# Kernel tuning notes

Hardware: AMD Instinct MI355X
Metric: run time of the kernel (lower is better)

Reference implementation:

```python
import jax, jax.numpy as jnp
import numpy as np

B, P, D = 8, 196, 768       # batch, patches per image, hidden
H, DH = 12, 64              # heads, head dim (H*DH == D)
L = 4                       # GAT layers
THRESH = 0.1                # GraphGenerator similarity threshold
SLOPE = 0.2                 # LeakyReLU negative slope (DGL GATConv default)
NEG = -1e9


def setup_inputs() -> dict:
    key = jax.random.key(0)
    k0, k1, k2, k3, k4 = jax.random.split(key, 5)
    l_feat = jax.random.normal(k0, (B, P, D), jnp.float32)
    r_feat = jax.random.normal(k1, (B, P, D), jnp.float32)
    W = jax.random.normal(k2, (L, D, H * DH), jnp.float32) / np.float32(np.sqrt(D))
    a_src = jax.random.normal(k3, (L, H, DH), jnp.float32) / np.float32(np.sqrt(DH))
    a_dst = jax.random.normal(k4, (L, H, DH), jnp.float32) / np.float32(np.sqrt(DH))
    b = jnp.zeros((L, H * DH), jnp.float32)
    return dict(l_feat=l_feat, r_feat=r_feat, W=W, a_src=a_src, a_dst=a_dst, b=b)


def _leaky(x):
    return jax.nn.leaky_relu(x, SLOPE)


def _gat_layer_bipartite(h, Wl, a_s, a_d, bias, mask_rl, Nl):
    # Graph: edges l->r where mask_rl[r, l] is True, plus a self loop on every node.
    # l-nodes therefore only see themselves (alpha = 1).
    N = h.shape[0]
    z = (h @ Wl).reshape(N, H, DH)                      # [N, H, DH]
    el = jnp.einsum('nhd,hd->nh', z, a_s)               # src score
    er = jnp.einsum('nhd,hd->nh', z, a_d)               # dst score
    zl, zr = z[:Nl], z[Nl:]
    cross = _leaky(el[:Nl][None, :, :] + er[Nl:][:, None, :])   # [Nr, Nl, H]
    cross = jnp.where(mask_rl[..., None], cross, NEG)
    self_r = _leaky(el[Nl:] + er[Nl:])                   # [Nr, H] self-loop logit
    logits = jnp.concatenate([cross, self_r[:, None, :]], axis=1)  # [Nr, Nl+1, H]
    alpha = jax.nn.softmax(logits, axis=1)
    out_r = jnp.einsum('rlh,lhd->rhd', alpha[:, :Nl], zl) + alpha[:, Nl][..., None] * zr
    out = jnp.concatenate([zl, out_r], axis=0)           # l-nodes: identity (self loop)
    return out.reshape(N, H * DH) + bias


def _gat_layer_pool(h, Wl, a_s, a_d, bias):
    # Graph from _gather: every node -> first node of its P-block (col = img_node
    # repeat_interleave) plus add_self_loop. The root's self edge thus appears TWICE,
    # giving it multiplicity 2 in the edge softmax. Non-root nodes: self loop only.
    N = h.shape[0]
    G = N // P
    z = (h @ Wl).reshape(G, P, H, DH)
    el = jnp.einsum('gphd,hd->gph', z, a_s)
    er = jnp.einsum('gphd,hd->gph', z, a_d)
    logits = _leaky(el + er[:, :1, :])                   # [G, P, H], dst = node 0
    logc = jnp.log(jnp.where(jnp.arange(P) == 0, 2.0, 1.0)).astype(h.dtype)
    alpha = jax.nn.softmax(logits + logc[None, :, None], axis=1)
    pooled = jnp.einsum('gph,gphd->ghd', alpha, z)       # root aggregation
    out = z.at[:, 0].set(pooled)                         # others keep self value
    return out.reshape(N, H * DH) + bias


def _gat(h, W, a_src, a_dst, b, layer_fn):
    for i in range(L):
        h = layer_fn(h, W[i], a_src[i], a_dst[i], b[i])
        if i < L - 1:
            h = jax.nn.elu(h)
    return h


def reference(l_feat, r_feat, W, a_src, a_dst, b):
    node_l = l_feat.reshape(-1, D)
    node_r = r_feat.reshape(-1, D)
    Nl = node_l.shape[0]
    # GraphGenerator: cosine-similarity threshold graph (edges l -> r)
    nl = node_l / jnp.linalg.norm(node_l, axis=-1, keepdims=True)
    nr = node_r / jnp.linalg.norm(node_r, axis=-1, keepdims=True)
    mask_rl = (nr @ nl.T) > THRESH                       # [Nr, Nl]
    h = jnp.concatenate([node_l, node_r], axis=0)        # [2*B*P, D]
    h = _gat(h, W, a_src, a_dst, b,
             lambda x, w, s, d, bb: _gat_layer_bipartite(x, w, s, d, bb, mask_rl, Nl))
    # second GAT pass on the pooling graph, then index_select the per-image roots
    h = _gat(h, W, a_src, a_dst, b, _gat_layer_pool)
    img = h[::P]                                         # img_node = arange(0, N, P)
    return img[:B], img[B:]                              # (node_feat_l, node_feat_r)
```

## Files before the change

kernel.cpp:

```cpp
#include <hip/hip_runtime.h>
#include <math.h>

#define NL    1568
#define NTOT  3136
#define DD    768
#define NH    12
#define DHD   64
#define WPR   49
#define MAXDEG 64
#define NKSTEP 24
#define LOG2F_ 0.69314718055994530942f

typedef _Float16 h8 __attribute__((ext_vector_type(8)));
typedef float f32x4 __attribute__((ext_vector_type(4)));
#define MFMA16(a, b, c) __builtin_amdgcn_mfma_f32_16x16x32_f16(a, b, c, 0, 0, 0)

__device__ __forceinline__ float leaky(float x) { return x > 0.f ? x : 0.2f * x; }

__device__ __forceinline__ void gld16(const _Float16* g, _Float16* l) {
  __builtin_amdgcn_global_load_lds(
      (const __attribute__((address_space(1))) void*)g,
      (__attribute__((address_space(3))) void*)l, 16, 0, 0);
}

__global__ __launch_bounds__(192) void conv_init(const float* __restrict__ lf, const float* __restrict__ rf,
                                                 _Float16* __restrict__ hi, _Float16* __restrict__ lo,
                                                 float* __restrict__ norms) {
  int n = blockIdx.x;
  int t = threadIdx.x;
  const float* src = (n < NL) ? lf + (size_t)n * DD : rf + (size_t)(n - NL) * DD;
  float4 v = reinterpret_cast<const float4*>(src)[t];
  _Float16 a0 = (_Float16)v.x, a1 = (_Float16)v.y, a2 = (_Float16)v.z, a3 = (_Float16)v.w;
  typedef _Float16 h4v __attribute__((ext_vector_type(4)));
  h4v hv = {a0, a1, a2, a3};
  h4v lv = {(_Float16)((v.x - (float)a0) * 2048.f), (_Float16)((v.y - (float)a1) * 2048.f),
            (_Float16)((v.z - (float)a2) * 2048.f), (_Float16)((v.w - (float)a3) * 2048.f)};
  size_t idx = (size_t)n * (DD / 4) + t;
  reinterpret_cast<h4v*>(hi)[idx] = hv;
  reinterpret_cast<h4v*>(lo)[idx] = lv;
  float s = v.x * v.x + v.y * v.y + v.z * v.z + v.w * v.w;
  #pragma unroll
  for (int o = 32; o; o >>= 1) s += __shfl_xor(s, o);
  __shared__ float red[3];
  if ((t & 63) == 0) red[t >> 6] = s;
  __syncthreads();
  if (t == 0) norms[n] = sqrtf(red[0] + red[1] + red[2]);
}

__global__ __launch_bounds__(256) void transp_W(const float* __restrict__ W, _Float16* __restrict__ Wthi) {
  __shared__ float tile[32][33];
  int kt = blockIdx.x * 32, nt = blockIdx.y * 32, i = blockIdx.z;
  int tx = threadIdx.x & 31, ty = threadIdx.x >> 5;
  const float* Wp = W + ((size_t)i * DD + kt) * DD + nt;
  #pragma unroll
  for (int p = 0; p < 4; ++p) tile[ty + p * 8][tx] = Wp[(size_t)(ty + p * 8) * DD + tx];
  __syncthreads();
  _Float16* oh = Wthi + ((size_t)i * DD + nt) * DD + kt;
  #pragma unroll
  for (int p = 0; p < 4; ++p) {
    int nn = ty + p * 8;
    oh[(size_t)nn * DD + tx] = (_Float16)tile[tx][nn];
  }
}

__global__ __launch_bounds__(256) void gemm_mfma(const _Float16* __restrict__ Ahi,
                                                 const _Float16* __restrict__ Bhi,
                                                 const float* __restrict__ a_s, const float* __restrict__ a_d,
                                                 const float* __restrict__ bias, float* __restrict__ C,
                                                 float* __restrict__ el, float* __restrict__ er,
                                                 _Float16* __restrict__ ohhi,
                                                 int do_elu, int mode) {
  __shared__ _Float16 sm[2][2][2048];
  int t = threadIdx.x;
  int xcd = blockIdx.x & 7, pos = blockIdx.x >> 3;
  int orig = (xcd < 4 ? xcd * 74 : 4 * 74 + (xcd - 4) * 73) + pos;
  int bx = orig / 12, by = orig % 12;
  int m0 = bx * 64, n0 = by * 64;

  int rl = t >> 2;
  int kq_src = (t & 3) ^ ((t >> 3) & 3);
  size_t aoff = (size_t)(m0 + rl) * DD + kq_src * 8;
  size_t boff = (size_t)(n0 + rl) * DD + kq_src * 8;
  const _Float16* pAhi = Ahi + aoff;
  const _Float16* pBhi = Bhi + boff;
  int ch = (t >> 6) * 512;

  int ln = t & 63, wv = t >> 6;
  int fr = ln & 15, kg = ln >> 4;
  int kq8 = (kg ^ ((fr >> 1) & 3)) * 8;
  int aRead = (wv * 16 + fr) * 32 + kq8;

  f32x4 zero = {0.f, 0.f, 0.f, 0.f};
  f32x4 acc1[4];
  #pragma unroll
  for (int cg = 0; cg < 4; ++cg) acc1[cg] = zero;

  gld16(pAhi, &sm[0][0][ch]);
  gld16(pBhi, &sm[0][1][ch]);
  __syncthreads();

  for (int step = 0; step < NKSTEP; ++step) {
    int buf = step & 1;
    if (step < NKSTEP - 1) {
      int kb = (step + 1) * 32;
      gld16(pAhi + kb, &sm[buf ^ 1][0][ch]);
      gld16(pBhi + kb, &sm[buf ^ 1][1][ch]);
    }
    h8 ah = *reinterpret_cast<const h8*>(&sm[buf][0][aRead]);
    #pragma unroll
    for (int cg = 0; cg < 4; ++cg) {
      int bRead = (cg * 16 + fr) * 32 + kq8;
      h8 bh = *reinterpret_cast<const h8*>(&sm[buf][1][bRead]);
      acc1[cg] = MFMA16(ah, bh, acc1[cg]);
    }
    __syncthreads();
  }

  int head = by;
  int orow = m0 + wv * 16 + kg * 4;
  #pragma unroll
  for (int i = 0; i < 4; ++i) {
    int r = orow + i;
    bool wh = (mode == 0) ? (r < NL) : (r % 196 != 0);
    #pragma unroll
    for (int cg = 0; cg < 4; ++cg) {
      int c = n0 + cg * 16 + fr;
      float z = acc1[cg][i];
      C[(size_t)r * DD + c] = z;
      if (wh) {
        float o = z + bias[c];
        if (do_elu) o = o > 0.f ? o : expm1f(o);
        ohhi[(size_t)r * DD + c] = (_Float16)o;
      }
    }
  }
  float asv[4], adv[4];
  #pragma unroll
  for (int cg = 0; cg < 4; ++cg) {
    asv[cg] = a_s[head * DHD + cg * 16 + fr];
    adv[cg] = a_d[head * DHD + cg * 16 + fr];
  }
  #pragma unroll
  for (int i = 0; i < 4; ++i) {
    float s1 = 0.f, s2 = 0.f;
    #pragma unroll
    for (int cg = 0; cg < 4; ++cg) {
      s1 = fmaf(acc1[cg][i], asv[cg], s1);
      s2 = fmaf(acc1[cg][i], adv[cg], s2);
    }
    #pragma unroll
    for (int o = 1; o < 16; o <<= 1) {
      s1 += __shfl_xor(s1, o);
      s2 += __shfl_xor(s2, o);
    }
    if (fr == 0) {
      el[(size_t)(orow + i) * NH + head] = s1;
      er[(size_t)(orow + i) * NH + head] = s2;
    }
  }
}

__global__ __launch_bounds__(256) void mask_mfma(const _Float16* __restrict__ Hhi, const _Float16* __restrict__ Hlo,
                                                 const float* __restrict__ norms, unsigned* __restrict__ mask) {
  __shared__ _Float16 sm[2][4][2048];
  __shared__ unsigned mw[64][2];
  int t = threadIdx.x;
  int r0 = blockIdx.x * 64, l0 = blockIdx.y * 64;

  int rl = t >> 2;
  int kq_src = (t & 3) ^ ((t >> 3) & 3);
  int ra = r0 + rl; if (ra >= NL) ra = NL - 1;
  int la = l0 + rl; if (la >= NL) la = NL - 1;
  size_t aoff = (size_t)(NL + ra) * DD + kq_src * 8;
  size_t boff = (size_t)la * DD + kq_src * 8;
  const _Float16* pAhi = Hhi + aoff;
  const _Float16* pAlo = Hlo + aoff;
  const _Float16* pBhi = Hhi + boff;
  const _Float16* pBlo = Hlo + boff;
  int ch = (t >> 6) * 512;

  int ln = t & 63, wv = t >> 6;
  int fr = ln & 15, kg = ln >> 4;
  int kq8 = (kg ^ ((fr >> 1) & 3)) * 8;
  int aRead = (wv * 16 + fr) * 32 + kq8;

  f32x4 zero = {0.f, 0.f, 0.f, 0.f};
  f32x4 acc1[4], acc2[4];
  #pragma unroll
  for (int cg = 0; cg < 4; ++cg) { acc1[cg] = zero; acc2[cg] = zero; }
  if (t < 128) mw[t >> 1][t & 1] = 0u;

  gld16(pAhi, &sm[0][0][ch]);
  gld16(pAlo, &sm[0][1][ch]);
  gld16(pBhi, &sm[0][2][ch]);
  gld16(pBlo, &sm[0][3][ch]);
  __syncthreads();

  for (int step = 0; step < NKSTEP; ++step) {
    int buf = step & 1;
    if (step < NKSTEP - 1) {
      int kb = (step + 1) * 32;
      gld16(pAhi + kb, &sm[buf ^ 1][0][ch]);
      gld16(pAlo + kb, &sm[buf ^ 1][1][ch]);
      gld16(pBhi + kb, &sm[buf ^ 1][2][ch]);
      gld16(pBlo + kb, &sm[buf ^ 1][3][ch]);
    }
    h8 ah = *reinterpret_cast<const h8*>(&sm[buf][0][aRead]);
    h8 al = *reinterpret_cast<const h8*>(&sm[buf][1][aRead]);
    #pragma unroll
    for (int cg = 0; cg < 4; ++cg) {
      int bRead = (cg * 16 + fr) * 32 + kq8;
      h8 bh = *reinterpret_cast<const h8*>(&sm[buf][2][bRead]);
      h8 bl = *reinterpret_cast<const h8*>(&sm[buf][3][bRead]);
      acc1[cg] = MFMA16(ah, bh, acc1[cg]);
      acc2[cg] = MFMA16(ah, bl, acc2[cg]);
      acc2[cg] = MFMA16(al, bh, acc2[cg]);
    }
    __syncthreads();
  }

  int rloc = wv * 16 + kg * 4;
  float nrv[4];
  #pragma unroll
  for (int i = 0; i < 4; ++i) {
    int r = r0 + rloc + i;
    nrv[i] = norms[NL + (r < NL ? r : NL - 1)];
  }
  #pragma unroll
  for (int cg = 0; cg < 4; ++cg) {
    int lloc = cg * 16 + fr;
    int l = l0 + lloc;
    float nlv = norms[l < NL ? l : NL - 1];
    #pragma unroll
    for (int i = 0; i < 4; ++i) {
      int r = r0 + rloc + i;
      float dot = acc1[cg][i] + acc2[cg][i] * (1.f / 2048.f);
      if (r < NL && l < NL && dot > 0.1f * nrv[i] * nlv)
        atomicOr(&mw[rloc + i][lloc >> 5], 1u << (lloc & 31));
    }
  }
  __syncthreads();
  if (t < 128) {
    int rr = t >> 1, w = t & 1;
    int rg = r0 + rr, wg = blockIdx.y * 2 + w;
    if (rg < NL && wg < WPR) mask[(size_t)rg * WPR + wg] = mw[rr][w];
  }
}

__global__ __launch_bounds__(64) void build_csr(const unsigned* __restrict__ mask,
                                                int* __restrict__ nbr, int* __restrict__ deg) {
  int r = blockIdx.x * 64 + threadIdx.x;
  if (r >= NL) return;
  const unsigned* mr = mask + (size_t)r * WPR;
  int* out = nbr + (size_t)r * MAXDEG;
  int cnt = 0;
  #pragma unroll 7
  for (int w = 0; w < WPR; ++w) {
    unsigned m = mr[w];
    while (m) {
      int bpos = __ffs(m) - 1;
      m &= m - 1;
      if (cnt < MAXDEG) out[cnt] = w * 32 + bpos;
      ++cnt;
    }
  }
  deg[r] = cnt < MAXDEG ? cnt : MAXDEG;
}

__global__ __launch_bounds__(768) void bip_fused(const float* __restrict__ z, const float* __restrict__ el,
                                                 const float* __restrict__ er, const int* __restrict__ nbr,
                                                 const int* __restrict__ deg, const float* __restrict__ bias,
                                                 _Float16* __restrict__ ohhi,
                                                 int do_elu) {
  int r = blockIdx.x;
  int R = NL + r;
  int t = threadIdx.x;
  int dg = deg[r];
  __shared__ int nb_s[MAXDEG];
  __shared__ float wbuf[MAXDEG * NH];
  __shared__ float den_s[NH], wself_s[NH];
  if (t < dg) nb_s[t] = nbr[(size_t)r * MAXDEG + t];
  __syncthreads();
  if (t < dg * NH) {
    int j = t / NH, h2 = t - j * NH;
    wbuf[t] = el[(size_t)nb_s[j] * NH + h2];
  }
  __syncthreads();
  if (t < NH) {
    float er_r = er[(size_t)R * NH + t];
    float s = leaky(el[(size_t)R * NH + t] + er_r);
    float mx = s;
    for (int j = 0; j < dg; ++j) mx = fmaxf(mx, leaky(wbuf[j * NH + t] + er_r));
    float den = 0.f;
    for (int j = 0; j < dg; ++j) {
      float w = expf(leaky(wbuf[j * NH + t] + er_r) - mx);
      wbuf[j * NH + t] = w;
      den += w;
    }
    float ws = expf(s - mx);
    den_s[t] = den + ws;
    wself_s[t] = ws;
  }
  __syncthreads();
  int h2 = t >> 6;
  float acc = wself_s[h2] * z[(size_t)R * DD + t];
  for (int j = 0; j < dg; ++j)
    acc = fmaf(wbuf[j * NH + h2], z[(size_t)nb_s[j] * DD + t], acc);
  float o = acc / den_s[h2] + bias[t];
  if (do_elu) o = o > 0.f ? o : expm1f(o);
  ohhi[(size_t)R * DD + t] = (_Float16)o;
}

__global__ __launch_bounds__(256) void pool_attn2(const float* __restrict__ z, const float* __restrict__ el,
                                                  const float* __restrict__ er, const float* __restrict__ bias,
                                                  _Float16* __restrict__ ohhi,
                                                  float* __restrict__ root_out, int do_elu) {
  int g = blockIdx.x, h = blockIdx.y;
  int base = g * 196;
  int t = threadIdx.x;
  int w = t >> 6, d = t & 63;
  __shared__ float wb[196];
  __shared__ float red[4];
  __shared__ float accP[4][64];
  float er0 = er[(size_t)base * NH + h];
  float lg = -INFINITY;
  if (t < 196) {
    lg = leaky(el[(size_t)(base + t) * NH + h] + er0);
    if (t == 0) lg += LOG2F_;
  }
  float m = lg;
  #pragma unroll
  for (int o = 32; o; o >>= 1) m = fmaxf(m, __shfl_xor(m, o));
  if ((t & 63) == 0) red[w] = m;
  __syncthreads();
  float mx = fmaxf(fmaxf(red[0], red[1]), fmaxf(red[2], red[3]));
  float wgt = (t < 196) ? expf(lg - mx) : 0.f;
  if (t < 196) wb[t] = wgt;
  float dn = wgt;
  #pragma unroll
  for (int o = 32; o; o >>= 1) dn += __shfl_xor(dn, o);
  __syncthreads();
  if ((t & 63) == 0) red[w] = dn;
  __syncthreads();
  float den = red[0] + red[1] + red[2] + red[3];
  float acc = 0.f;
  int p0 = w * 49;
  #pragma unroll 7
  for (int p = p0; p < p0 + 49; ++p)
    acc = fmaf(wb[p], z[(size_t)(base + p) * DD + h * DHD + d], acc);
  accP[w][d] = acc;
  __syncthreads();
  if (w == 0) {
    float o = (accP[0][d] + accP[1][d] + accP[2][d] + accP[3][d]) / den + bias[h * DHD + d];
    if (do_elu) o = o > 0.f ? o : expm1f(o);
    int c = h * DHD + d;
    ohhi[(size_t)base * DD + c] = (_Float16)o;
    root_out[(size_t)g * DD + c] = o;
  }
}

extern "C" void kernel_launch(void* const* d_in, const int* in_sizes, int n_in,
                              void* d_out, int out_size, void* d_ws, size_t ws_size,
                              hipStream_t stream) {
  const float* l_feat = (const float*)d_in[0];
  const float* r_feat = (const float*)d_in[1];
  const float* W      = (const float*)d_in[2];
  const float* a_src  = (const float*)d_in[3];
  const float* a_dst  = (const float*)d_in[4];
  const float* b      = (const float*)d_in[5];
  float* out = (float*)d_out;

  float* z     = (float*)d_ws;
  float* el    = z + (size_t)NTOT * DD;
  float* er    = el + (size_t)NTOT * NH;
  float* norms = er + (size_t)NTOT * NH;
  float* hroot = norms + NTOT;
  unsigned* mask = (unsigned*)(hroot + 16 * DD);
  int* nbr = (int*)(mask + (size_t)NL * WPR);
  int* deg = nbr + (size_t)NL * MAXDEG;
  _Float16* hhiA = (_Float16*)(deg + NL);
  _Float16* hloA = hhiA + (size_t)NTOT * DD;
  _Float16* hhiB = hloA + (size_t)NTOT * DD;
  _Float16* Wthi = hhiB + (size_t)NTOT * DD;

  _Float16* hhi[2] = {hhiA, hhiB};

  conv_init<<<NTOT, 192, 0, stream>>>(l_feat, r_feat, hhiA, hloA, norms);
  transp_W<<<dim3(24, 24, 4), 256, 0, stream>>>(W, Wthi);
  mask_mfma<<<dim3(25, 25), 256, 0, stream>>>(hhiA, hloA, norms, mask);
  build_csr<<<(NL + 63) / 64, 64, 0, stream>>>(mask, nbr, deg);

  for (int i = 0; i < 4; ++i) {
    const float* bi = b + (size_t)i * DD;
    int do_elu = (i < 3) ? 1 : 0;
    int ib = i & 1, ob = (i + 1) & 1;
    gemm_mfma<<<588, 256, 0, stream>>>(hhi[ib],
        Wthi + (size_t)i * DD * DD,
        a_src + (size_t)i * NH * DHD, a_dst + (size_t)i * NH * DHD,
        bi, z, el, er, hhi[ob], do_elu, 0);
    bip_fused<<<NL, 768, 0, stream>>>(z, el, er, nbr, deg, bi, hhi[ob], do_elu);
  }

  for (int i = 0; i < 4; ++i) {
    const float* bi = b + (size_t)i * DD;
    int do_elu = (i < 3) ? 1 : 0;
    int L = 4 + i;
    int ib = L & 1, ob = (L + 1) & 1;
    gemm_mfma<<<588, 256, 0, stream>>>(hhi[ib],
        Wthi + (size_t)i * DD * DD,
        a_src + (size_t)i * NH * DHD, a_dst + (size_t)i * NH * DHD,
        bi, z, el, er, hhi[ob], do_elu, 1);
    pool_attn2<<<dim3(16, NH), 256, 0, stream>>>(z, el, er, bi, hhi[ob],
        (i == 3) ? out : hroot, do_elu);
  }
}
```

Baseline: 274.9 us.

## Use 32x32 MFMA with 64x128 GEMM tiles and store z in fp16

The projection GEMM now uses 32x32x16 MFMA instructions on a 64x128 output tile per block, halving the grid to 294 blocks and reusing each A tile across two heads. The projected features z are written as fp16 instead of fp32, which halves the write and read traffic in bip_fused and pool_attn2. The trade-off is fewer blocks for 256 CUs and lower precision in the aggregated z values.

```diff
diff --git a/kernel.cpp b/kernel.cpp
--- a/kernel.cpp
+++ b/kernel.cpp
@@ -13,7 +13,9 @@
 
 typedef _Float16 h8 __attribute__((ext_vector_type(8)));
 typedef float f32x4 __attribute__((ext_vector_type(4)));
+typedef float f32x16 __attribute__((ext_vector_type(16)));
 #define MFMA16(a, b, c) __builtin_amdgcn_mfma_f32_16x16x32_f16(a, b, c, 0, 0, 0)
+#define MFMA32(a, b, c) __builtin_amdgcn_mfma_f32_32x32x16_f16(a, b, c, 0, 0, 0)
 
 __device__ __forceinline__ float leaky(float x) { return x > 0.f ? x : 0.2f * x; }
 
@@ -66,96 +68,100 @@
 __global__ __launch_bounds__(256) void gemm_mfma(const _Float16* __restrict__ Ahi,
                                                  const _Float16* __restrict__ Bhi,
                                                  const float* __restrict__ a_s, const float* __restrict__ a_d,
-                                                 const float* __restrict__ bias, float* __restrict__ C,
+                                                 const float* __restrict__ bias,
+                                                 _Float16* __restrict__ zh,
                                                  float* __restrict__ el, float* __restrict__ er,
                                                  _Float16* __restrict__ ohhi,
                                                  int do_elu, int mode) {
-  __shared__ _Float16 sm[2][2][2048];
+  __shared__ _Float16 smA[2][2048];
+  __shared__ _Float16 smB[2][4096];
   int t = threadIdx.x;
   int xcd = blockIdx.x & 7, pos = blockIdx.x >> 3;
-  int orig = (xcd < 4 ? xcd * 74 : 4 * 74 + (xcd - 4) * 73) + pos;
-  int bx = orig / 12, by = orig % 12;
-  int m0 = bx * 64, n0 = by * 64;
+  int orig = (xcd < 6 ? xcd * 37 : 222 + (xcd - 6) * 36) + pos;
+  int bx = orig / 6, by = orig % 6;
+  int m0 = bx * 64, n0 = by * 128;
 
   int rl = t >> 2;
-  int kq_src = (t & 3) ^ ((t >> 3) & 3);
-  size_t aoff = (size_t)(m0 + rl) * DD + kq_src * 8;
-  size_t boff = (size_t)(n0 + rl) * DD + kq_src * 8;
-  const _Float16* pAhi = Ahi + aoff;
-  const _Float16* pBhi = Bhi + boff;
-  int ch = (t >> 6) * 512;
-
-  int ln = t & 63, wv = t >> 6;
-  int fr = ln & 15, kg = ln >> 4;
-  int kq8 = (kg ^ ((fr >> 1) & 3)) * 8;
-  int aRead = (wv * 16 + fr) * 32 + kq8;
-
-  f32x4 zero = {0.f, 0.f, 0.f, 0.f};
-  f32x4 acc1[4];
-  #pragma unroll
-  for (int cg = 0; cg < 4; ++cg) acc1[cg] = zero;
-
-  gld16(pAhi, &sm[0][0][ch]);
-  gld16(pBhi, &sm[0][1][ch]);
+  int kq_src = (t & 3) ^ ((rl >> 1) & 3);
+  const _Float16* pA  = Ahi + (size_t)(m0 + rl) * DD + kq_src * 8;
+  const _Float16* pB1 = Bhi + (size_t)(n0 + rl) * DD + kq_src * 8;
+  const _Float16* pB2 = Bhi + (size_t)(n0 + 64 + rl) * DD + kq_src * 8;
+  int w = t >> 6, l = t & 63;
+  int chA  = w * 512;
+  int chB2 = 2048 + w * 512;
+
+  int cl = l & 31, hi = l >> 5;
+  int rw = (w >> 1) * 32, cw = (w & 1) * 64;
+  int arow = rw + cl;
+  int aOff0 = arow * 32 + ((hi)     ^ ((arow >> 1) & 3)) * 8;
+  int aOff1 = arow * 32 + ((hi + 2) ^ ((arow >> 1) & 3)) * 8;
+  int brow0 = cw + cl, brow1 = cw + 32 + cl;
+  int bOff00 = brow0 * 32 + ((hi)     ^ ((brow0 >> 1) & 3)) * 8;
+  int bOff01 = brow0 * 32 + ((hi + 2) ^ ((brow0 >> 1) & 3)) * 8;
+  int bOff10 = brow1 * 32 + ((hi)     ^ ((brow1 >> 1) & 3)) * 8;
+  int bOff11 = brow1 * 32 + ((hi + 2) ^ ((brow1 >> 1) & 3)) * 8;
+
+  f32x16 acc0, acc1;
+  #pragma unroll
+  for (int i = 0; i < 16; ++i) { acc0[i] = 0.f; acc1[i] = 0.f; }
+
+  gld16(pA,  &smA[0][chA]);
+  gld16(pB1, &smB[0][chA]);
+  gld16(pB2, &smB[0][chB2]);
   __syncthreads();
 
   for (int step = 0; step < NKSTEP; ++step) {
     int buf = step & 1;
     if (step < NKSTEP - 1) {
       int kb = (step + 1) * 32;
-      gld16(pAhi + kb, &sm[buf ^ 1][0][ch]);
-      gld16(pBhi + kb, &sm[buf ^ 1][1][ch]);
-    }
-    h8 ah = *reinterpret_cast<const h8*>(&sm[buf][0][aRead]);
+      gld16(pA + kb,  &smA[buf ^ 1][chA]);
+      gld16(pB1 + kb, &smB[buf ^ 1][chA]);
+      gld16(pB2 + kb, &smB[buf ^ 1][chB2]);
+    }
+    h8 a0  = *reinterpret_cast<const h8*>(&smA[buf][aOff0]);
+    h8 a1  = *reinterpret_cast<const h8*>(&smA[buf][aOff1]);
+    h8 b00 = *reinterpret_cast<const h8*>(&smB[buf][bOff00]);
+    h8 b01 = *reinterpret_cast<const h8*>(&smB[buf][bOff01]);
+    h8 b10 = *reinterpret_cast<const h8*>(&smB[buf][bOff10]);
+    h8 b11 = *reinterpret_cast<const h8*>(&smB[buf][bOff11]);
+    acc0 = MFMA32(a0, b00, acc0);
+    acc1 = MFMA32(a0, b10, acc1);
+    acc0 = MFMA32(a1, b01, acc0);
+    acc1 = MFMA32(a1, b11, acc1);
+    __syncthreads();
+  }
+
+  int hd = by * 2 + (w & 1);
+  float as0 = a_s[hd * DHD + cl],      ad0 = a_d[hd * DHD + cl];
+  float as1 = a_s[hd * DHD + 32 + cl], ad1 = a_d[hd * DHD + 32 + cl];
+  int c0 = n0 + cw + cl, c1 = c0 + 32;
+  float bv0 = bias[c0], bv1 = bias[c1];
+  #pragma unroll
+  for (int r = 0; r < 16; ++r) {
+    int row = m0 + rw + (r & 3) + 8 * (r >> 2) + 4 * hi;
+    float z0 = acc0[r], z1 = acc1[r];
+    zh[(size_t)row * DD + c0] = (_Float16)z0;
+    zh[(size_t)row * DD + c1] = (_Float16)z1;
+    bool wh = (mode == 0) ? (row < NL) : (row % 196 != 0);
+    if (wh) {
+      float o0 = z0 + bv0, o1 = z1 + bv1;
+      if (do_elu) {
+        o0 = o0 > 0.f ? o0 : expm1f(o0);
+        o1 = o1 > 0.f ? o1 : expm1f(o1);
+      }
+      ohhi[(size_t)row * DD + c0] = (_Float16)o0;
+      ohhi[(size_t)row * DD + c1] = (_Float16)o1;
+    }
+    float s1 = z0 * as0 + z1 * as1;
+    float s2 = z0 * ad0 + z1 * ad1;
     #pragma unroll
-    for (int cg = 0; cg < 4; ++cg) {
-      int bRead = (cg * 16 + fr) * 32 + kq8;
-      h8 bh = *reinterpret_cast<const h8*>(&sm[buf][1][bRead]);
-      acc1[cg] = MFMA16(ah, bh, acc1[cg]);
-    }
-    __syncthreads();
-  }
-
-  int head = by;
-  int orow = m0 + wv * 16 + kg * 4;
-  #pragma unroll
-  for (int i = 0; i < 4; ++i) {
-    int r = orow + i;
-    bool wh = (mode == 0) ? (r < NL) : (r % 196 != 0);
-    #pragma unroll
-    for (int cg = 0; cg < 4; ++cg) {
-      int c = n0 + cg * 16 + fr;
-      float z = acc1[cg][i];
-      C[(size_t)r * DD + c] = z;
-      if (wh) {
-        float o = z + bias[c];
-        if (do_elu) o = o > 0.f ? o : expm1f(o);
-        ohhi[(size_t)r * DD + c] = (_Float16)o;
-      }
-    }
-  }
-  float asv[4], adv[4];
-  #pragma unroll
-  for (int cg = 0; cg < 4; ++cg) {
-    asv[cg] = a_s[head * DHD + cg * 16 + fr];
-    adv[cg] = a_d[head * DHD + cg * 16 + fr];
-  }
-  #pragma unroll
-  for (int i = 0; i < 4; ++i) {
-    float s1 = 0.f, s2 = 0.f;
-    #pragma unroll
-    for (int cg = 0; cg < 4; ++cg) {
-      s1 = fmaf(acc1[cg][i], asv[cg], s1);
-      s2 = fmaf(acc1[cg][i], adv[cg], s2);
-    }
-    #pragma unroll
-    for (int o = 1; o < 16; o <<= 1) {
+    for (int o = 1; o < 32; o <<= 1) {
       s1 += __shfl_xor(s1, o);
       s2 += __shfl_xor(s2, o);
     }
-    if (fr == 0) {
-      el[(size_t)(orow + i) * NH + head] = s1;
-      er[(size_t)(orow + i) * NH + head] = s2;
+    if (cl == 0) {
+      el[(size_t)row * NH + hd] = s1;
+      er[(size_t)row * NH + hd] = s2;
     }
   }
 }
@@ -267,7 +273,7 @@
   deg[r] = cnt < MAXDEG ? cnt : MAXDEG;
 }
 
-__global__ __launch_bounds__(768) void bip_fused(const float* __restrict__ z, const float* __restrict__ el,
+__global__ __launch_bounds__(768) void bip_fused(const _Float16* __restrict__ zh, const float* __restrict__ el,
                                                  const float* __restrict__ er, const int* __restrict__ nbr,
                                                  const int* __restrict__ deg, const float* __restrict__ bias,
                                                  _Float16* __restrict__ ohhi,
@@ -303,15 +309,15 @@
   }
   __syncthreads();
   int h2 = t >> 6;
-  float acc = wself_s[h2] * z[(size_t)R * DD + t];
+  float acc = wself_s[h2] * (float)zh[(size_t)R * DD + t];
   for (int j = 0; j < dg; ++j)
-    acc = fmaf(wbuf[j * NH + h2], z[(size_t)nb_s[j] * DD + t], acc);
+    acc = fmaf(wbuf[j * NH + h2], (float)zh[(size_t)nb_s[j] * DD + t], acc);
   float o = acc / den_s[h2] + bias[t];
   if (do_elu) o = o > 0.f ? o : expm1f(o);
   ohhi[(size_t)R * DD + t] = (_Float16)o;
 }
 
-__global__ __launch_bounds__(256) void pool_attn2(const float* __restrict__ z, const float* __restrict__ el,
+__global__ __launch_bounds__(256) void pool_attn2(const _Float16* __restrict__ zh, const float* __restrict__ el,
                                                   const float* __restrict__ er, const float* __restrict__ bias,
                                                   _Float16* __restrict__ ohhi,
                                                   float* __restrict__ root_out, int do_elu) {
@@ -347,7 +353,7 @@
   int p0 = w * 49;
   #pragma unroll 7
   for (int p = p0; p < p0 + 49; ++p)
-    acc = fmaf(wb[p], z[(size_t)(base + p) * DD + h * DHD + d], acc);
+    acc = fmaf(wb[p], (float)zh[(size_t)(base + p) * DD + h * DHD + d], acc);
   accP[w][d] = acc;
   __syncthreads();
   if (w == 0) {
@@ -370,8 +376,7 @@
   const float* b      = (const float*)d_in[5];
   float* out = (float*)d_out;
 
-  float* z     = (float*)d_ws;
-  float* el    = z + (size_t)NTOT * DD;
+  float* el    = (float*)d_ws;
   float* er    = el + (size_t)NTOT * NH;
   float* norms = er + (size_t)NTOT * NH;
   float* hroot = norms + NTOT;
@@ -382,6 +387,7 @@
   _Float16* hloA = hhiA + (size_t)NTOT * DD;
   _Float16* hhiB = hloA + (size_t)NTOT * DD;
   _Float16* Wthi = hhiB + (size_t)NTOT * DD;
+  _Float16* zh   = Wthi + (size_t)4 * DD * DD;
 
   _Float16* hhi[2] = {hhiA, hhiB};
 
@@ -394,11 +400,11 @@
     const float* bi = b + (size_t)i * DD;
     int do_elu = (i < 3) ? 1 : 0;
     int ib = i & 1, ob = (i + 1) & 1;
-    gemm_mfma<<<588, 256, 0, stream>>>(hhi[ib],
+    gemm_mfma<<<294, 256, 0, stream>>>(hhi[ib],
         Wthi + (size_t)i * DD * DD,
         a_src + (size_t)i * NH * DHD, a_dst + (size_t)i * NH * DHD,
-        bi, z, el, er, hhi[ob], do_elu, 0);
-    bip_fused<<<NL, 768, 0, stream>>>(z, el, er, nbr, deg, bi, hhi[ob], do_elu);
+        bi, zh, el, er, hhi[ob], do_elu, 0);
+    bip_fused<<<NL, 768, 0, stream>>>(zh, el, er, nbr, deg, bi, hhi[ob], do_elu);
   }
 
   for (int i = 0; i < 4; ++i) {
@@ -406,11 +412,11 @@
     int do_elu = (i < 3) ? 1 : 0;
     int L = 4 + i;
     int ib = L & 1, ob = (L + 1) & 1;
-    gemm_mfma<<<588, 256, 0, stream>>>(hhi[ib],
+    gemm_mfma<<<294, 256, 0, stream>>>(hhi[ib],
         Wthi + (size_t)i * DD * DD,
         a_src + (size_t)i * NH * DHD, a_dst + (size_t)i * NH * DHD,
-        bi, z, el, er, hhi[ob], do_elu, 1);
-    pool_attn2<<<dim3(16, NH), 256, 0, stream>>>(z, el, er, bi, hhi[ob],
+        bi, zh, el, er, hhi[ob], do_elu, 1);
+    pool_attn2<<<dim3(16, NH), 256, 0, stream>>>(zh, el, er, bi, hhi[ob],
         (i == 3) ? out : hroot, do_elu);
   }
 }
```

After: 308.2 us. +12.1%, slower.

## Store projected features as fp16 and use 64-wide K tiles in GEMM

Applied to the files above, without the earlier changes.

The GEMM now loads 64-wide K slices per stage, with a new XOR swizzle, which halves the number of loop iterations and barriers. The projected feature matrix z is written in half precision instead of fp32. The bipartite and pooling attention kernels read this fp16 z, which halves the bytes written by the GEMM and gathered per neighbour. The trade-off is extra rounding error in z and higher LDS use per block.

```diff
diff --git a/kernel.cpp b/kernel.cpp
--- a/kernel.cpp
+++ b/kernel.cpp
@@ -9,6 +9,7 @@
 #define WPR   49
 #define MAXDEG 64
 #define NKSTEP 24
+#define NK64   12
 #define LOG2F_ 0.69314718055994530942f
 
 typedef _Float16 h8 __attribute__((ext_vector_type(8)));
@@ -66,58 +67,76 @@
 __global__ __launch_bounds__(256) void gemm_mfma(const _Float16* __restrict__ Ahi,
                                                  const _Float16* __restrict__ Bhi,
                                                  const float* __restrict__ a_s, const float* __restrict__ a_d,
-                                                 const float* __restrict__ bias, float* __restrict__ C,
+                                                 const float* __restrict__ bias,
+                                                 _Float16* __restrict__ zh,
                                                  float* __restrict__ el, float* __restrict__ er,
                                                  _Float16* __restrict__ ohhi,
                                                  int do_elu, int mode) {
-  __shared__ _Float16 sm[2][2][2048];
+  __shared__ _Float16 smA[2][4096];
+  __shared__ _Float16 smB[2][4096];
   int t = threadIdx.x;
   int xcd = blockIdx.x & 7, pos = blockIdx.x >> 3;
-  int orig = (xcd < 4 ? xcd * 74 : 4 * 74 + (xcd - 4) * 73) + pos;
+  int orig = (xcd < 4 ? xcd * 74 : 296 + (xcd - 4) * 73) + pos;
   int bx = orig / 12, by = orig % 12;
   int m0 = bx * 64, n0 = by * 64;
 
-  int rl = t >> 2;
-  int kq_src = (t & 3) ^ ((t >> 3) & 3);
-  size_t aoff = (size_t)(m0 + rl) * DD + kq_src * 8;
-  size_t boff = (size_t)(n0 + rl) * DD + kq_src * 8;
-  const _Float16* pAhi = Ahi + aoff;
-  const _Float16* pBhi = Bhi + boff;
-  int ch = (t >> 6) * 512;
-
-  int ln = t & 63, wv = t >> 6;
-  int fr = ln & 15, kg = ln >> 4;
-  int kq8 = (kg ^ ((fr >> 1) & 3)) * 8;
-  int aRead = (wv * 16 + fr) * 32 + kq8;
+  int rs = t >> 3;
+  int kq0 = (t & 7) ^ (rs & 7);
+  const _Float16* pA0 = Ahi + (size_t)(m0 + rs) * DD + kq0 * 8;
+  const _Float16* pA1 = pA0 + (size_t)32 * DD;
+  const _Float16* pB0 = Bhi + (size_t)(n0 + rs) * DD + kq0 * 8;
+  const _Float16* pB1 = pB0 + (size_t)32 * DD;
+  int w = t >> 6, l = t & 63;
+  int ch0 = w * 512;
+  int ch1 = 2048 + w * 512;
+
+  int fr = l & 15, kg = l >> 4;
+  int aO[2], bO[4][2];
+  #pragma unroll
+  for (int kk = 0; kk < 2; ++kk) {
+    int arow = w * 16 + fr;
+    aO[kk] = arow * 64 + (((kk * 4 + kg) ^ (arow & 7)) * 8);
+    #pragma unroll
+    for (int cg = 0; cg < 4; ++cg) {
+      int brow = cg * 16 + fr;
+      bO[cg][kk] = brow * 64 + (((kk * 4 + kg) ^ (brow & 7)) * 8);
+    }
+  }
 
   f32x4 zero = {0.f, 0.f, 0.f, 0.f};
-  f32x4 acc1[4];
-  #pragma unroll
-  for (int cg = 0; cg < 4; ++cg) acc1[cg] = zero;
-
-  gld16(pAhi, &sm[0][0][ch]);
-  gld16(pBhi, &sm[0][1][ch]);
-  __syncthreads();
-
-  for (int step = 0; step < NKSTEP; ++step) {
+  f32x4 acc[4];
+  #pragma unroll
+  for (int cg = 0; cg < 4; ++cg) acc[cg] = zero;
+
+  gld16(pA0, &smA[0][ch0]);
+  gld16(pA1, &smA[0][ch1]);
+  gld16(pB0, &smB[0][ch0]);
+  gld16(pB1, &smB[0][ch1]);
+  __syncthreads();
+
+  for (int step = 0; step < NK64; ++step) {
     int buf = step & 1;
-    if (step < NKSTEP - 1) {
-      int kb = (step + 1) * 32;
-      gld16(pAhi + kb, &sm[buf ^ 1][0][ch]);
-      gld16(pBhi + kb, &sm[buf ^ 1][1][ch]);
-    }
-    h8 ah = *reinterpret_cast<const h8*>(&sm[buf][0][aRead]);
-    #pragma unroll
-    for (int cg = 0; cg < 4; ++cg) {
-      int bRead = (cg * 16 + fr) * 32 + kq8;
-      h8 bh = *reinterpret_cast<const h8*>(&sm[buf][1][bRead]);
-      acc1[cg] = MFMA16(ah, bh, acc1[cg]);
+    if (step < NK64 - 1) {
+      int kb = (step + 1) * 64;
+      gld16(pA0 + kb, &smA[buf ^ 1][ch0]);
+      gld16(pA1 + kb, &smA[buf ^ 1][ch1]);
+      gld16(pB0 + kb, &smB[buf ^ 1][ch0]);
+      gld16(pB1 + kb, &smB[buf ^ 1][ch1]);
+    }
+    #pragma unroll
+    for (int kk = 0; kk < 2; ++kk) {
+      h8 a = *reinterpret_cast<const h8*>(&smA[buf][aO[kk]]);
+      #pragma unroll
+      for (int cg = 0; cg < 4; ++cg) {
+        h8 b = *reinterpret_cast<const h8*>(&smB[buf][bO[cg][kk]]);
+        acc[cg] = MFMA16(a, b, acc[cg]);
+      }
     }
     __syncthreads();
   }
 
   int head = by;
-  int orow = m0 + wv * 16 + kg * 4;
+  int orow = m0 + w * 16 + kg * 4;
   #pragma unroll
   for (int i = 0; i < 4; ++i) {
     int r = orow + i;
@@ -125,8 +144,8 @@
     #pragma unroll
     for (int cg = 0; cg < 4; ++cg) {
       int c = n0 + cg * 16 + fr;
-      float z = acc1[cg][i];
-      C[(size_t)r * DD + c] = z;
+      float z = acc[cg][i];
+      zh[(size_t)r * DD + c] = (_Float16)z;
       if (wh) {
         float o = z + bias[c];
         if (do_elu) o = o > 0.f ? o : expm1f(o);
@@ -145,8 +164,8 @@
     float s1 = 0.f, s2 = 0.f;
     #pragma unroll
     for (int cg = 0; cg < 4; ++cg) {
-      s1 = fmaf(acc1[cg][i], asv[cg], s1);
-      s2 = fmaf(acc1[cg][i], adv[cg], s2);
+      s1 = fmaf(acc[cg][i], asv[cg], s1);
+      s2 = fmaf(acc[cg][i], adv[cg], s2);
     }
     #pragma unroll
     for (int o = 1; o < 16; o <<= 1) {
@@ -267,7 +286,7 @@
   deg[r] = cnt < MAXDEG ? cnt : MAXDEG;
 }
 
-__global__ __launch_bounds__(768) void bip_fused(const float* __restrict__ z, const float* __restrict__ el,
+__global__ __launch_bounds__(768) void bip_fused(const _Float16* __restrict__ zh, const float* __restrict__ el,
                                                  const float* __restrict__ er, const int* __restrict__ nbr,
                                                  const int* __restrict__ deg, const float* __restrict__ bias,
                                                  _Float16* __restrict__ ohhi,
@@ -303,15 +322,15 @@
   }
   __syncthreads();
   int h2 = t >> 6;
-  float acc = wself_s[h2] * z[(size_t)R * DD + t];
+  float acc = wself_s[h2] * (float)zh[(size_t)R * DD + t];
   for (int j = 0; j < dg; ++j)
-    acc = fmaf(wbuf[j * NH + h2], z[(size_t)nb_s[j] * DD + t], acc);
+    acc = fmaf(wbuf[j * NH + h2], (float)zh[(size_t)nb_s[j] * DD + t], acc);
   float o = acc / den_s[h2] + bias[t];
   if (do_elu) o = o > 0.f ? o : expm1f(o);
   ohhi[(size_t)R * DD + t] = (_Float16)o;
 }
 
-__global__ __launch_bounds__(256) void pool_attn2(const float* __restrict__ z, const float* __restrict__ el,
+__global__ __launch_bounds__(256) void pool_attn2(const _Float16* __restrict__ zh, const float* __restrict__ el,
                                                   const float* __restrict__ er, const float* __restrict__ bias,
                                                   _Float16* __restrict__ ohhi,
                                                   float* __restrict__ root_out, int do_elu) {
@@ -347,7 +366,7 @@
   int p0 = w * 49;
   #pragma unroll 7
   for (int p = p0; p < p0 + 49; ++p)
-    acc = fmaf(wb[p], z[(size_t)(base + p) * DD + h * DHD + d], acc);
+    acc = fmaf(wb[p], (float)zh[(size_t)(base + p) * DD + h * DHD + d], acc);
   accP[w][d] = acc;
   __syncthreads();
   if (w == 0) {
@@ -370,8 +389,7 @@
   const float* b      = (const float*)d_in[5];
   float* out = (float*)d_out;
 
-  float* z     = (float*)d_ws;
-  float* el    = z + (size_t)NTOT * DD;
+  float* el    = (float*)d_ws;
   float* er    = el + (size_t)NTOT * NH;
   float* norms = er + (size_t)NTOT * NH;
   float* hroot = norms + NTOT;
@@ -382,6 +400,7 @@
   _Float16* hloA = hhiA + (size_t)NTOT * DD;
   _Float16* hhiB = hloA + (size_t)NTOT * DD;
   _Float16* Wthi = hhiB + (size_t)NTOT * DD;
+  _Float16* zh   = Wthi + (size_t)4 * DD * DD;
 
   _Float16* hhi[2] = {hhiA, hhiB};
 
@@ -397,8 +416,8 @@
     gemm_mfma<<<588, 256, 0, stream>>>(hhi[ib],
         Wthi + (size_t)i * DD * DD,
         a_src + (size_t)i * NH * DHD, a_dst + (size_t)i * NH * DHD,
-        bi, z, el, er, hhi[ob], do_elu, 0);
-    bip_fused<<<NL, 768, 0, stream>>>(z, el, er, nbr, deg, bi, hhi[ob], do_elu);
+        bi, zh, el, er, hhi[ob], do_elu, 0);
+    bip_fused<<<NL, 768, 0, stream>>>(zh, el, er, nbr, deg, bi, hhi[ob], do_elu);
   }
 
   for (int i = 0; i < 4; ++i) {
@@ -409,8 +428,8 @@
     gemm_mfma<<<588, 256, 0, stream>>>(hhi[ib],
         Wthi + (size_t)i * DD * DD,
         a_src + (size_t)i * NH * DHD, a_dst + (size_t)i * NH * DHD,
-        bi, z, el, er, hhi[ob], do_elu, 1);
-    pool_attn2<<<dim3(16, NH), 256, 0, stream>>>(z, el, er, bi, hhi[ob],
+        bi, zh, el, er, hhi[ob], do_elu, 1);
+    pool_attn2<<<dim3(16, NH), 256, 0, stream>>>(zh, el, er, bi, hhi[ob],
         (i == 3) ? out : hroot, do_elu);
   }
 }
```

Result: slower. 281.1 us (+2.3%).

## Store GAT projections in fp16 and use single-pass fp16 mask with fp32 fallback

Applied to the files above, without the earlier changes.

The similarity-mask GEMM now uses only the fp16 high part instead of the hi/lo split, which halves its MFMA and load work. Pairs whose fp16 dot product lands within 0.5 of the threshold are recomputed exactly in fp32 straight from the input features. Separately, the projected features z are stored as fp16 instead of fp32, which halves the write traffic in the GEMM and the gather traffic in the attention kernels. The cost is lower precision in the aggregated outputs, and a fallback path whose per-element work varies and can diverge within a wavefront.

```diff
diff --git a/kernel.cpp b/kernel.cpp
--- a/kernel.cpp
+++ b/kernel.cpp
@@ -24,20 +24,14 @@
 }
 
 __global__ __launch_bounds__(192) void conv_init(const float* __restrict__ lf, const float* __restrict__ rf,
-                                                 _Float16* __restrict__ hi, _Float16* __restrict__ lo,
-                                                 float* __restrict__ norms) {
+                                                 _Float16* __restrict__ hi, float* __restrict__ norms) {
   int n = blockIdx.x;
   int t = threadIdx.x;
   const float* src = (n < NL) ? lf + (size_t)n * DD : rf + (size_t)(n - NL) * DD;
   float4 v = reinterpret_cast<const float4*>(src)[t];
-  _Float16 a0 = (_Float16)v.x, a1 = (_Float16)v.y, a2 = (_Float16)v.z, a3 = (_Float16)v.w;
   typedef _Float16 h4v __attribute__((ext_vector_type(4)));
-  h4v hv = {a0, a1, a2, a3};
-  h4v lv = {(_Float16)((v.x - (float)a0) * 2048.f), (_Float16)((v.y - (float)a1) * 2048.f),
-            (_Float16)((v.z - (float)a2) * 2048.f), (_Float16)((v.w - (float)a3) * 2048.f)};
-  size_t idx = (size_t)n * (DD / 4) + t;
-  reinterpret_cast<h4v*>(hi)[idx] = hv;
-  reinterpret_cast<h4v*>(lo)[idx] = lv;
+  h4v hv = {(_Float16)v.x, (_Float16)v.y, (_Float16)v.z, (_Float16)v.w};
+  reinterpret_cast<h4v*>(hi)[(size_t)n * (DD / 4) + t] = hv;
   float s = v.x * v.x + v.y * v.y + v.z * v.z + v.w * v.w;
   #pragma unroll
   for (int o = 32; o; o >>= 1) s += __shfl_xor(s, o);
@@ -66,14 +60,15 @@
 __global__ __launch_bounds__(256) void gemm_mfma(const _Float16* __restrict__ Ahi,
                                                  const _Float16* __restrict__ Bhi,
                                                  const float* __restrict__ a_s, const float* __restrict__ a_d,
-                                                 const float* __restrict__ bias, float* __restrict__ C,
+                                                 const float* __restrict__ bias,
+                                                 _Float16* __restrict__ zh,
                                                  float* __restrict__ el, float* __restrict__ er,
                                                  _Float16* __restrict__ ohhi,
                                                  int do_elu, int mode) {
   __shared__ _Float16 sm[2][2][2048];
   int t = threadIdx.x;
   int xcd = blockIdx.x & 7, pos = blockIdx.x >> 3;
-  int orig = (xcd < 4 ? xcd * 74 : 4 * 74 + (xcd - 4) * 73) + pos;
+  int orig = (xcd < 4 ? xcd * 74 : 296 + (xcd - 4) * 73) + pos;
   int bx = orig / 12, by = orig % 12;
   int m0 = bx * 64, n0 = by * 64;
 
@@ -91,9 +86,9 @@
   int aRead = (wv * 16 + fr) * 32 + kq8;
 
   f32x4 zero = {0.f, 0.f, 0.f, 0.f};
-  f32x4 acc1[4];
-  #pragma unroll
-  for (int cg = 0; cg < 4; ++cg) acc1[cg] = zero;
+  f32x4 acc[4];
+  #pragma unroll
+  for (int cg = 0; cg < 4; ++cg) acc[cg] = zero;
 
   gld16(pAhi, &sm[0][0][ch]);
   gld16(pBhi, &sm[0][1][ch]);
@@ -111,7 +106,7 @@
     for (int cg = 0; cg < 4; ++cg) {
       int bRead = (cg * 16 + fr) * 32 + kq8;
       h8 bh = *reinterpret_cast<const h8*>(&sm[buf][1][bRead]);
-      acc1[cg] = MFMA16(ah, bh, acc1[cg]);
+      acc[cg] = MFMA16(ah, bh, acc[cg]);
     }
     __syncthreads();
   }
@@ -125,8 +120,8 @@
     #pragma unroll
     for (int cg = 0; cg < 4; ++cg) {
       int c = n0 + cg * 16 + fr;
-      float z = acc1[cg][i];
-      C[(size_t)r * DD + c] = z;
+      float z = acc[cg][i];
+      zh[(size_t)r * DD + c] = (_Float16)z;
       if (wh) {
         float o = z + bias[c];
         if (do_elu) o = o > 0.f ? o : expm1f(o);
@@ -145,8 +140,8 @@
     float s1 = 0.f, s2 = 0.f;
     #pragma unroll
     for (int cg = 0; cg < 4; ++cg) {
-      s1 = fmaf(acc1[cg][i], asv[cg], s1);
-      s2 = fmaf(acc1[cg][i], adv[cg], s2);
+      s1 = fmaf(acc[cg][i], asv[cg], s1);
+      s2 = fmaf(acc[cg][i], adv[cg], s2);
     }
     #pragma unroll
     for (int o = 1; o < 16; o <<= 1) {
@@ -160,9 +155,10 @@
   }
 }
 
-__global__ __launch_bounds__(256) void mask_mfma(const _Float16* __restrict__ Hhi, const _Float16* __restrict__ Hlo,
+__global__ __launch_bounds__(256) void mask_mfma(const _Float16* __restrict__ Hhi,
+                                                 const float* __restrict__ lf, const float* __restrict__ rf,
                                                  const float* __restrict__ norms, unsigned* __restrict__ mask) {
-  __shared__ _Float16 sm[2][4][2048];
+  __shared__ _Float16 sm[2][2][2048];
   __shared__ unsigned mw[64][2];
   int t = threadIdx.x;
   int r0 = blockIdx.x * 64, l0 = blockIdx.y * 64;
@@ -171,12 +167,8 @@
   int kq_src = (t & 3) ^ ((t >> 3) & 3);
   int ra = r0 + rl; if (ra >= NL) ra = NL - 1;
   int la = l0 + rl; if (la >= NL) la = NL - 1;
-  size_t aoff = (size_t)(NL + ra) * DD + kq_src * 8;
-  size_t boff = (size_t)la * DD + kq_src * 8;
-  const _Float16* pAhi = Hhi + aoff;
-  const _Float16* pAlo = Hlo + aoff;
-  const _Float16* pBhi = Hhi + boff;
-  const _Float16* pBlo = Hlo + boff;
+  const _Float16* pA = Hhi + (size_t)(NL + ra) * DD + kq_src * 8;
+  const _Float16* pB = Hhi + (size_t)la * DD + kq_src * 8;
   int ch = (t >> 6) * 512;
 
   int ln = t & 63, wv = t >> 6;
@@ -185,36 +177,28 @@
   int aRead = (wv * 16 + fr) * 32 + kq8;
 
   f32x4 zero = {0.f, 0.f, 0.f, 0.f};
-  f32x4 acc1[4], acc2[4];
-  #pragma unroll
-  for (int cg = 0; cg < 4; ++cg) { acc1[cg] = zero; acc2[cg] = zero; }
+  f32x4 acc[4];
+  #pragma unroll
+  for (int cg = 0; cg < 4; ++cg) acc[cg] = zero;
   if (t < 128) mw[t >> 1][t & 1] = 0u;
 
-  gld16(pAhi, &sm[0][0][ch]);
-  gld16(pAlo, &sm[0][1][ch]);
-  gld16(pBhi, &sm[0][2][ch]);
-  gld16(pBlo, &sm[0][3][ch]);
+  gld16(pA, &sm[0][0][ch]);
+  gld16(pB, &sm[0][1][ch]);
   __syncthreads();
 
   for (int step = 0; step < NKSTEP; ++step) {
     int buf = step & 1;
     if (step < NKSTEP - 1) {
       int kb = (step + 1) * 32;
-      gld16(pAhi + kb, &sm[buf ^ 1][0][ch]);
-      gld16(pAlo + kb, &sm[buf ^ 1][1][ch]);
-      gld16(pBhi + kb, &sm[buf ^ 1][2][ch]);
-      gld16(pBlo + kb, &sm[buf ^ 1][3][ch]);
+      gld16(pA + kb, &sm[buf ^ 1][0][ch]);
+      gld16(pB + kb, &sm[buf ^ 1][1][ch]);
     }
     h8 ah = *reinterpret_cast<const h8*>(&sm[buf][0][aRead]);
-    h8 al = *reinterpret_cast<const h8*>(&sm[buf][1][aRead]);
     #pragma unroll
     for (int cg = 0; cg < 4; ++cg) {
       int bRead = (cg * 16 + fr) * 32 + kq8;
-      h8 bh = *reinterpret_cast<const h8*>(&sm[buf][2][bRead]);
-      h8 bl = *reinterpret_cast<const h8*>(&sm[buf][3][bRead]);
-      acc1[cg] = MFMA16(ah, bh, acc1[cg]);
-      acc2[cg] = MFMA16(ah, bl, acc2[cg]);
-      acc2[cg] = MFMA16(al, bh, acc2[cg]);
+      h8 bh = *reinterpret_cast<const h8*>(&sm[buf][1][bRead]);
+      acc[cg] = MFMA16(ah, bh, acc[cg]);
     }
     __syncthreads();
   }
@@ -234,9 +218,25 @@
     #pragma unroll
     for (int i = 0; i < 4; ++i) {
       int r = r0 + rloc + i;
-      float dot = acc1[cg][i] + acc2[cg][i] * (1.f / 2048.f);
-      if (r < NL && l < NL && dot > 0.1f * nrv[i] * nlv)
-        atomicOr(&mw[rloc + i][lloc >> 5], 1u << (lloc & 31));
+      if (r >= NL || l >= NL) continue;
+      float thr = 0.1f * nrv[i] * nlv;
+      float dot = acc[cg][i];
+      bool bit;
+      if (fabsf(dot - thr) <= 0.5f) {
+        const float4* rp = reinterpret_cast<const float4*>(rf + (size_t)r * DD);
+        const float4* lp = reinterpret_cast<const float4*>(lf + (size_t)l * DD);
+        float s = 0.f;
+        #pragma unroll 4
+        for (int k = 0; k < DD / 4; ++k) {
+          float4 a = rp[k], b = lp[k];
+          s = fmaf(a.x, b.x, s); s = fmaf(a.y, b.y, s);
+          s = fmaf(a.z, b.z, s); s = fmaf(a.w, b.w, s);
+        }
+        bit = s > thr;
+      } else {
+        bit = dot > thr;
+      }
+      if (bit) atomicOr(&mw[rloc + i][lloc >> 5], 1u << (lloc & 31));
     }
   }
   __syncthreads();
@@ -267,7 +267,7 @@
   deg[r] = cnt < MAXDEG ? cnt : MAXDEG;
 }
 
-__global__ __launch_bounds__(768) void bip_fused(const float* __restrict__ z, const float* __restrict__ el,
+__global__ __launch_bounds__(768) void bip_fused(const _Float16* __restrict__ zh, const float* __restrict__ el,
                                                  const float* __restrict__ er, const int* __restrict__ nbr,
                                                  const int* __restrict__ deg, const float* __restrict__ bias,
                                                  _Float16* __restrict__ ohhi,
@@ -303,15 +303,15 @@
   }
   __syncthreads();
   int h2 = t >> 6;
-  float acc = wself_s[h2] * z[(size_t)R * DD + t];
+  float acc = wself_s[h2] * (float)zh[(size_t)R * DD + t];
   for (int j = 0; j < dg; ++j)
-    acc = fmaf(wbuf[j * NH + h2], z[(size_t)nb_s[j] * DD + t], acc);
+    acc = fmaf(wbuf[j * NH + h2], (float)zh[(size_t)nb_s[j] * DD + t], acc);
   float o = acc / den_s[h2] + bias[t];
   if (do_elu) o = o > 0.f ? o : expm1f(o);
   ohhi[(size_t)R * DD + t] = (_Float16)o;
 }
 
-__global__ __launch_bounds__(256) void pool_attn2(const float* __restrict__ z, const float* __restrict__ el,
+__global__ __launch_bounds__(256) void pool_attn2(const _Float16* __restrict__ zh, const float* __restrict__ el,
                                                   const float* __restrict__ er, const float* __restrict__ bias,
                                                   _Float16* __restrict__ ohhi,
                                                   float* __restrict__ root_out, int do_elu) {
@@ -347,7 +347,7 @@
   int p0 = w * 49;
   #pragma unroll 7
   for (int p = p0; p < p0 + 49; ++p)
-    acc = fmaf(wb[p], z[(size_t)(base + p) * DD + h * DHD + d], acc);
+    acc = fmaf(wb[p], (float)zh[(size_t)(base + p) * DD + h * DHD + d], acc);
   accP[w][d] = acc;
   __syncthreads();
   if (w == 0) {
@@ -370,8 +370,7 @@
   const float* b      = (const float*)d_in[5];
   float* out = (float*)d_out;
 
-  float* z     = (float*)d_ws;
-  float* el    = z + (size_t)NTOT * DD;
+  float* el    = (float*)d_ws;
   float* er    = el + (size_t)NTOT * NH;
   float* norms = er + (size_t)NTOT * NH;
   float* hroot = norms + NTOT;
@@ -379,15 +378,15 @@
   int* nbr = (int*)(mask + (size_t)NL * WPR);
   int* deg = nbr + (size_t)NL * MAXDEG;
   _Float16* hhiA = (_Float16*)(deg + NL);
-  _Float16* hloA = hhiA + (size_t)NTOT * DD;
-  _Float16* hhiB = hloA + (size_t)NTOT * DD;
+  _Float16* hhiB = hhiA + (size_t)NTOT * DD;
   _Float16* Wthi = hhiB + (size_t)NTOT * DD;
+  _Float16* zh   = Wthi + (size_t)4 * DD * DD;
 
   _Float16* hhi[2] = {hhiA, hhiB};
 
-  conv_init<<<NTOT, 192, 0, stream>>>(l_feat, r_feat, hhiA, hloA, norms);
+  conv_init<<<NTOT, 192, 0, stream>>>(l_feat, r_feat, hhiA, norms);
   transp_W<<<dim3(24, 24, 4), 256, 0, stream>>>(W, Wthi);
-  mask_mfma<<<dim3(25, 25), 256, 0, stream>>>(hhiA, hloA, norms, mask);
+  mask_mfma<<<dim3(25, 25), 256, 0, stream>>>(hhiA, l_feat, r_feat, norms, mask);
   build_csr<<<(NL + 63) / 64, 64, 0, stream>>>(mask, nbr, deg);
 
   for (int i = 0; i < 4; ++i) {
@@ -397,8 +396,8 @@
     gemm_mfma<<<588, 256, 0, stream>>>(hhi[ib],
         Wthi + (size_t)i * DD * DD,
         a_src + (size_t)i * NH * DHD, a_dst + (size_t)i * NH * DHD,
-        bi, z, el, er, hhi[ob], do_elu, 0);
-    bip_fused<<<NL, 768, 0, stream>>>(z, el, er, nbr, deg, bi, hhi[ob], do_elu);
+        bi, zh, el, er, hhi[ob], do_elu, 0);
+    bip_fused<<<NL, 768, 0, stream>>>(zh, el, er, nbr, deg, bi, hhi[ob], do_elu);
   }
 
   for (int i = 0; i < 4; ++i) {
@@ -409,8 +408,8 @@
     gemm_mfma<<<588, 256, 0, stream>>>(hhi[ib],
         Wthi + (size_t)i * DD * DD,
         a_src + (size_t)i * NH * DHD, a_dst + (size_t)i * NH * DHD,
-        bi, z, el, er, hhi[ob], do_elu, 1);
-    pool_attn2<<<dim3(16, NH), 256, 0, stream>>>(z, el, er, bi, hhi[ob],
+        bi, zh, el, er, hhi[ob], do_elu, 1);
+    pool_attn2<<<dim3(16, NH), 256, 0, stream>>>(zh, el, er, bi, hhi[ob],
         (i == 3) ? out : hroot, do_elu);
   }
 }
```

Result: slower. 289.1 us (+5.2%).
